# Kernel optimization log

Hardware: AMD Instinct MI355X
Metric: run time of the kernel (lower is better)

Reference implementation:

```python
import jax, jax.numpy as jnp
import numpy as np

T, B, IN, H, E = 100, 1, 36, 256, 2048


def setup_inputs() -> dict:
    key = jax.random.key(0)
    ks = jax.random.split(key, 18)
    rn = lambda k, shape, s=1.0: jax.random.normal(k, shape, jnp.float32) * s
    return dict(
        Y=rn(ks[0], (T, B, IN)),
        h0=rn(ks[1], (1, B, H)),
        c0=rn(ks[2], (1, B, H)),
        outEncoder=rn(ks[3], (E, H), 0.1),
        W_ih=rn(ks[4], (4 * H, IN), 0.1),
        W_hh=rn(ks[5], (4 * H, H), 0.1),
        b_ih=rn(ks[6], (4 * H,), 0.1),
        b_hh=rn(ks[7], (4 * H,), 0.1),
        att_W=rn(ks[8], (H, H), 0.1),
        att_V=rn(ks[9], (H, H), 0.1),
        att_b=rn(ks[10], (H, 1), 0.1),
        att_vector=rn(ks[11], (1, H), 0.1),
        W1=rn(ks[12], (H, 2 * H), 0.1),
        b1=rn(ks[13], (H,), 0.1),
        W2=rn(ks[14], (H, H), 0.1),
        b2=rn(ks[15], (H,), 0.1),
        W3=rn(ks[16], (IN, H), 0.1),
        b3=rn(ks[17], (IN,), 0.1),
    )


def reference(Y, h0, c0, outEncoder, W_ih, W_hh, b_ih, b_hh,
              att_W, att_V, att_b, att_vector, W1, b1, W2, b2, W3, b3):
    h = jnp.squeeze(h0, 0)  # [B,H]
    c = jnp.squeeze(c0, 0)  # [B,H]
    # VOut = att_V @ outEncoder^T is timestep-invariant: precompute. [H,E]
    VOut = att_V @ outEncoder.T

    def step(carry, y):
        h, c = carry  # h: [B,H], c: [B,H] (context from prev step after step 0)
        gates = y @ W_ih.T + b_ih + h @ W_hh.T + b_hh  # [B,4H]
        i_g, f_g, g_g, o_g = jnp.split(gates, 4, axis=1)
        cLSTM = jax.nn.sigmoid(f_g) * c + jax.nn.sigmoid(i_g) * jnp.tanh(g_g)
        h_new = jax.nn.sigmoid(o_g) * jnp.tanh(cLSTM)  # [B,H]
        # additive attention: hidden expanded to every encoder position
        WS = att_W @ h_new.T  # [H,1], broadcasts over E columns
        Escore = jnp.tanh(WS + VOut + att_b)  # [H,E]
        scores = att_vector @ Escore  # [1,E]
        alpha = jax.nn.softmax(scores, axis=-1)  # [1,E]
        ctx = alpha @ outEncoder  # [1,H]
        # MLP on concat(new cell state, context)
        v = jnp.concatenate([cLSTM, ctx], axis=1)  # [1,2H]
        v = jax.nn.relu(v @ W1.T + b1)
        v = jax.nn.relu(v @ W2.T + b2)
        out = v @ W3.T + b3  # [1,36]
        # NB: original feeds the attention context back as the LSTM cell state
        return (h_new, ctx), out

    (_, c_final), outputs = jax.lax.scan(step, (h, c), Y)
    return outputs, c_final  # outputs: [100,1,36]
```

## Files before the change

### kernel.cpp

```cpp
#include <hip/hip_runtime.h>
#include <stdint.h>


static constexpr float    L2E = 1.44269504088896341f;
static constexpr float    K2  = 2.88539008177792681f;
static constexpr unsigned SPIN_LIMIT = 200000u;

static constexpr size_t OFF_BC   = 0;
static constexpr size_t OFF_YG   = 524288;
static constexpr size_t OFF_GRAW = 626688;
static constexpr size_t OFF_CRAW = 729088;
static constexpr size_t CRAW_CP  = 25600;
static constexpr size_t OFF_STOT = 831488;
static constexpr size_t OFF_CLH  = 831616;
static constexpr size_t OFF_V1   = 857216;
static constexpr size_t OFF_V2   = 882816;
static constexpr size_t OFF_SYNC = 908416;

__device__ __forceinline__ float exp2fast(float x){ return __builtin_amdgcn_exp2f(x); }
__device__ __forceinline__ float rcpfast(float x){ return __builtin_amdgcn_rcpf(x); }
__device__ __forceinline__ float sigf(float x){ return rcpfast(1.f + exp2fast(-x*L2E)); }
__device__ __forceinline__ float tanhfast(float x){
  float E = exp2fast(x*K2);
  return 1.f - 2.f*rcpfast(E + 1.f);
}
__device__ __forceinline__ unsigned short f2bf(float f){
  unsigned b = __float_as_uint(f);
  return (unsigned short)((b + 0x7FFFu + ((b>>16)&1u))>>16);
}
__device__ __forceinline__ float bf2f(unsigned short u){ return __uint_as_float(((unsigned)u)<<16); }

__device__ __forceinline__ void gstore(float* p, float v){
  __hip_atomic_store(p, v, __ATOMIC_RELAXED, __HIP_MEMORY_SCOPE_AGENT);
}
__device__ __forceinline__ float gload(const float* p){
  return __hip_atomic_load(p, __ATOMIC_RELAXED, __HIP_MEMORY_SCOPE_AGENT);
}
__device__ __forceinline__ void gstore_u32(unsigned* p, unsigned v){
  __hip_atomic_store(p, v, __ATOMIC_RELAXED, __HIP_MEMORY_SCOPE_AGENT);
}
__device__ __forceinline__ unsigned gload_u32(const unsigned* p){
  return __hip_atomic_load(p, __ATOMIC_RELAXED, __HIP_MEMORY_SCOPE_AGENT);
}
__device__ __forceinline__ void gatomic_addf(float* p, float v){
  (void)__hip_atomic_fetch_add(p, v, __ATOMIC_RELAXED, __HIP_MEMORY_SCOPE_AGENT);
}

__device__ __forceinline__ void fbar(unsigned* flags, int w, unsigned ep){
  asm volatile("s_waitcnt vmcnt(0)" ::: "memory");
  __syncthreads();
  if (threadIdx.x == 0) gstore_u32(&flags[w], ep);
  if (threadIdx.x < 64) {
    int lane = threadIdx.x;
    unsigned it = 0;
    for (;;) {
      unsigned v = (lane < 32) ? gload_u32(&flags[lane]) : ep;
      if (__all((int)(v >= ep))) break;
      if (++it > SPIN_LIMIT) break;
    }
  }
  __syncthreads();
}
__device__ __forceinline__ void fwait_sleep(unsigned* flags, unsigned ep){
  if (threadIdx.x < 64) {
    int lane = threadIdx.x;
    unsigned it = 0;
    for (;;) {
      unsigned v = (lane < 32) ? gload_u32(&flags[lane]) : ep;
      if (__all((int)(v >= ep))) break;
      __builtin_amdgcn_s_sleep(2);
      if (++it > SPIN_LIMIT) break;
    }
  }
  __syncthreads();
}
__device__ __forceinline__ void arrive_cnt(unsigned* cnt){
  asm volatile("s_waitcnt vmcnt(0)" ::: "memory");
  __syncthreads();
  if (threadIdx.x == 0)
    __hip_atomic_fetch_add(cnt, 1u, __ATOMIC_RELAXED, __HIP_MEMORY_SCOPE_AGENT);
}
__device__ __forceinline__ void poll_ge(unsigned* p, unsigned tgt){
  if (threadIdx.x == 0){
    unsigned it = 0;
    while (gload_u32(p) < tgt){
      __builtin_amdgcn_s_sleep(2);
      if (++it > SPIN_LIMIT) break;
    }
  }
  __syncthreads();
}

__global__ __launch_bounds__(256) void rnn_prep(
    const float* __restrict__ Y, const float* __restrict__ h0,
    const float* __restrict__ outE, const float* __restrict__ W_ih,
    const float* __restrict__ W_hh, const float* __restrict__ b_ih,
    const float* __restrict__ b_hh, const float* __restrict__ att_V,
    const float* __restrict__ att_b, float* __restrict__ ws)
{
  __shared__ float avT[32*257];
  __shared__ float oeL[8*257];
  __shared__ float yL[40];
  __shared__ float h0L[256];
  const int b = blockIdx.x, tid = threadIdx.x;
  float* ws_bc   = ws + OFF_BC;
  float* ws_yg   = ws + OFF_YG;
  float* ws_graw = ws + OFF_GRAW;

  if (b < 256) {
    int e0 = b*8;
    for (int r=0;r<8;r++) oeL[r*257 + tid] = outE[(size_t)(e0+r)*256 + tid];
    int hl = tid & 31, er = tid >> 5;
    for (int ht=0; ht<8; ++ht) {
      __syncthreads();
      for (int i=0;i<32;i++){ int lin = tid + i*256; int r = lin>>8, j = lin&255;
        avT[r*257 + j] = att_V[(size_t)(ht*32+r)*256 + j]; }
      __syncthreads();
      float acc = 0.f;
      for (int j=0;j<256;j++) acc = fmaf(avT[hl*257 + j], oeL[er*257 + j], acc);
      int h = ht*32 + hl;
      ws_bc[(size_t)(e0+er)*256 + h] = (acc + att_b[h]) * K2;
    }
  } else if (b < 260) {
    int g = b - 256;
    for (int u=0; u<25; ++u) {
      int t = g*25 + u;
      __syncthreads();
      if (tid < 36) yL[tid] = Y[t*36 + tid];
      __syncthreads();
      for (int q=0;q<4;q++){
        int i = tid + 256*q;
        float acc = b_ih[i] + b_hh[i];
        for (int j=0;j<36;j++) acc = fmaf(W_ih[(size_t)i*36 + j], yL[j], acc);
        ws_yg[(size_t)t*1024 + i] = acc;
      }
    }
  } else if (b < 292) {
    int s = b - 260;
    if (tid < 256) h0L[tid] = h0[tid];
    if (tid < 36)  yL[tid]  = Y[tid];
    __syncthreads();
    int r = tid>>3, l8 = tid&7;
    int R = s*32 + r;
    float acc = 0.f;
    for (int q=0;q<32;q++){ int j = l8*32 + q; acc = fmaf(W_hh[(size_t)R*256 + j], h0L[j], acc); }
    acc += __shfl_xor(acc,1); acc += __shfl_xor(acc,2); acc += __shfl_xor(acc,4);
    if (l8 == 0){
      float full = acc + b_ih[R] + b_hh[R];
      for (int j=0;j<36;j++) full = fmaf(W_ih[(size_t)R*36 + j], yL[j], full);
      ws_graw[R] = full;
    }
  } else if (b == 292) {
    unsigned* s0 = (unsigned*)(ws + OFF_SYNC);
    gstore_u32(&s0[tid], 0u); gstore_u32(&s0[tid + 256], 0u);
  } else if (b == 293) {
    if (tid < 128) gstore(&ws[OFF_STOT + tid], 0.f);
  } else {
    int t = b - 294;
    #pragma unroll
    for (int c=0;c<4;c++)
      gstore(&ws[OFF_CRAW + (size_t)c*CRAW_CP + (size_t)t*256 + tid], 0.f);
  }
}

__global__ __launch_bounds__(512, 2) void rnn_main(
    const float* __restrict__ c0, const float* __restrict__ outE,
    const float* __restrict__ W_hh, const float* __restrict__ att_W,
    const float* __restrict__ att_vec,
    const float* __restrict__ W1, const float* __restrict__ b1,
    const float* __restrict__ W2, const float* __restrict__ b2,
    const float* __restrict__ W3, const float* __restrict__ b3,
    float* __restrict__ out, float* __restrict__ ws)
{
  __shared__ __align__(16) unsigned char smem[140288];
  const int w = blockIdx.x;
  const int tid = threadIdx.x;

  float* ws_yg    = ws + OFF_YG;
  float* ws_graw  = ws + OFF_GRAW;
  float* ws_craw  = ws + OFF_CRAW;
  float* ws_stot  = ws + OFF_STOT;
  float* ws_clh   = ws + OFF_CLH;
  float* ws_v1    = ws + OFF_V1;
  float* ws_v2    = ws + OFF_V2;
  unsigned* flags = (unsigned*)(ws + OFF_SYNC);
  unsigned* fv1   = flags + 64;
  unsigned* fv2   = flags + 192;

  if (w < 32) {
    float*          bcS    = (float*)(smem);
    unsigned short* oeS    = (unsigned short*)(smem + 67584);
    float*          whhS   = (float*)(smem + 100352);
    float*          wsS    = (float*)(smem + 133632);
    float*          hS     = (float*)(smem + 134688);
    float*          scoreS = (float*)(smem + 135712);
    float*          wexpS  = (float*)(smem + 135968);
    float*          pS     = (float*)(smem + 136224);
    float*          avS    = (float*)(smem + 138272);
    float*          stS    = (float*)(smem + 139328);

    unsigned awP[64];
    { int r = tid>>1, p = tid&1;
      const float* arow = att_W + (size_t)r*256 + p*128;
      #pragma unroll
      for (int q=0;q<64;q++){
        unsigned lo = f2bf(arow[2*q]);
        unsigned hi = f2bf(arow[2*q+1]);
        awP[q] = lo | (hi<<16);
      } }
    float Vpart = 0.f;
    { int l8 = tid & 7;
      #pragma unroll
      for (int k=0;k<32;k++) Vpart += att_vec[l8*32 + k]; }

    const float* ws_bc = ws + OFF_BC;
    for (int i=0;i<32;i++){ int lin = tid + i*512; int col = lin>>8, h = lin&255;
      bcS[col*264 + h + (h>>5)] = ws_bc[(size_t)(w*64+col)*256 + h]; }
    for (int i=0;i<32;i++){ int lin = tid + i*512; int col = lin>>8, h = lin&255;
      oeS[col*256 + h] = f2bf(outE[(size_t)(w*64+col)*256 + h]); }
    for (int i=0;i<16;i++){ int lin = tid + i*512; int r = lin>>8, j = lin&255;
      whhS[r*260 + j] = W_hh[(size_t)(w*32+r)*256 + j]; }
    if (tid < 256) avS[tid + (tid>>5)] = -2.f * att_vec[tid];
    __syncthreads();

    for (int t = 0; t < 100; ++t) {
      float ig, fg, gg, og;
      float cr0, cr1, cr2, cr3, st;
      if (tid < 256) {
        const float* g = ws_graw + (size_t)t*1024;
        ig = gload(&g[tid]);     fg = gload(&g[256+tid]);
        gg = gload(&g[512+tid]); og = gload(&g[768+tid]);
        if (t > 0) {
          const float* cb = ws_craw + (size_t)(t-1)*256 + tid;
          cr0 = gload(cb);             cr1 = gload(cb + CRAW_CP);
          cr2 = gload(cb + 2*CRAW_CP); cr3 = gload(cb + 3*CRAW_CP);
          st  = gload(&ws_stot[t-1]);
        }
      }
      if (tid < 256) {
        float c;
        if (t == 0) c = c0[tid];
        else        c = ((cr0+cr1)+(cr2+cr3)) * rcpfast(st);
        float cl = sigf(fg)*c + sigf(ig)*tanhfast(gg);
        float hn = sigf(og)*tanhfast(cl);
        hS[tid] = hn;
        if (w == 0) gstore(&ws_clh[(size_t)t*256 + tid], cl);
      }
      __syncthreads();
      { int r = tid>>1, p = tid&1;
        const float4* h4 = (const float4*)(hS + p*128);
        float acc = 0.f;
        #pragma unroll
        for (int i=0;i<32;i++){
          float4 hv = h4[i];
          unsigned pk0 = awP[2*i], pk1 = awP[2*i+1];
          acc = fmaf(__uint_as_float(pk0<<16),          hv.x, acc);
          acc = fmaf(__uint_as_float(pk0 & 0xffff0000u), hv.y, acc);
          acc = fmaf(__uint_as_float(pk1<<16),          hv.z, acc);
          acc = fmaf(__uint_as_float(pk1 & 0xffff0000u), hv.w, acc);
        }
        acc += __shfl_xor(acc, 1);
        if (p == 0) wsS[r + (r>>5)] = acc * K2; }
      __syncthreads();
      { int col = tid >> 3, l8 = tid & 7;
        const float* bcR = bcS + col*264 + l8*33;
        const float* wsR = wsS + l8*33;
        const float* avR = avS + l8*33;
        float acc = Vpart;
        #pragma unroll
        for (int k=0;k<32;k++){
          float E = exp2fast(bcR[k] + wsR[k]);
          acc = fmaf(avR[k], rcpfast(E + 1.f), acc);
        }
        acc += __shfl_xor(acc,1); acc += __shfl_xor(acc,2); acc += __shfl_xor(acc,4);
        if (l8 == 0) scoreS[col] = acc; }
      __syncthreads();
      if (tid < 64) {
        float ev = exp2fast(scoreS[tid] * L2E);
        wexpS[tid] = ev;
        float s = ev;
        #pragma unroll
        for (int d=1; d<64; d<<=1) s += __shfl_xor(s, d);
        if (tid == 0) gatomic_addf(&ws_stot[t], s);
      }
      __syncthreads();
      { int h = tid & 255, half = tid >> 8;
        float accp = 0.f;
        #pragma unroll
        for (int i=0;i<32;i++){ int lc = half*32 + i;
          accp = fmaf(wexpS[lc], bf2f(oeS[lc*256 + h]), accp); }
        pS[half*256 + h] = accp; }
      __syncthreads();
      if (tid < 256)
        gatomic_addf(&ws_craw[(size_t)(w>>3)*CRAW_CP + (size_t)t*256 + tid],
                     pS[tid] + pS[256 + tid]);
      if (t <= 98) {
        int r32 = tid >> 4, l16 = tid & 15;
        float acc2 = 0.f;
        #pragma unroll
        for (int q=0;q<16;q++){ int j = l16 + 16*q; acc2 = fmaf(whhS[r32*260 + j], hS[j], acc2); }
        acc2 += __shfl_xor(acc2,1); acc2 += __shfl_xor(acc2,2);
        acc2 += __shfl_xor(acc2,4); acc2 += __shfl_xor(acc2,8);
        if (l16 == 0){ int R = w*32 + r32;
          gstore(&ws_graw[(size_t)(t+1)*1024 + R], acc2 + ws_yg[(size_t)(t+1)*1024 + R]); }
      }
      fbar(flags, w, (unsigned)(t+1));
    }
    if (w == 0 && tid < 256) {
      const float* cb = ws_craw + (size_t)99*256 + tid;
      float rsum = (gload(cb) + gload(cb + CRAW_CP))
                 + (gload(cb + 2*CRAW_CP) + gload(cb + 3*CRAW_CP));
      out[3600 + tid] = rsum * rcpfast(gload(&ws_stot[99]));
    }
  } else if (w < 36) {
    float* wmS = (float*)(smem);
    float* vbS = (float*)(smem + 133632);
    int m = w - 32;
    for (int i=0;i<64;i++){ int lin = tid + i*512; int r = lin>>9, k = lin&511;
      wmS[r*520 + k + (k>>6)] = W1[(size_t)(m*64+r)*512 + k]; }
    __syncthreads();
    for (int s=0; s<100; ++s){
      fwait_sleep(flags, (unsigned)(s+1));
      { float val;
        if (tid < 256) val = gload(&ws_clh[(size_t)s*256 + tid]);
        else {
          const float* cb = ws_craw + (size_t)s*256 + (tid-256);
          float rsum = (gload(cb) + gload(cb + CRAW_CP))
                     + (gload(cb + 2*CRAW_CP) + gload(cb + 3*CRAW_CP));
          val = rsum * rcpfast(gload(&ws_stot[s]));
        }
        vbS[tid + (tid>>6)] = val; }
      __syncthreads();
      int row = tid >> 3, l8 = tid & 7;
      const float* wr = wmS + row*520 + l8*65;
      const float* vr = vbS + l8*65;
      float acc = 0.f;
      #pragma unroll
      for (int q=0;q<64;q++) acc = fmaf(wr[q], vr[q], acc);
      acc += __shfl_xor(acc,1); acc += __shfl_xor(acc,2); acc += __shfl_xor(acc,4);
      if (l8 == 0){ int i = m*64 + row; gstore(&ws_v1[(size_t)s*256 + i], fmaxf(acc + b1[i], 0.f)); }
      arrive_cnt(&fv1[s]);
      __syncthreads();
    }
  } else if (w < 38) {
    float* wmS = (float*)(smem);
    float* vbS = (float*)(smem + 133632);
    int m = w - 36;
    for (int i=0;i<64;i++){ int lin = tid + i*512; int r = lin>>8, k = lin&255;
      wmS[r*260 + k + (k>>6)] = W2[(size_t)(m*128+r)*256 + k]; }
    __syncthreads();
    for (int s=0; s<100; ++s){
      poll_ge(&fv1[s], 4u);
      if (tid < 256) vbS[tid + (tid>>6)] = gload(&ws_v1[(size_t)s*256 + tid]);
      __syncthreads();
      int row = tid >> 2, l4 = tid & 3;
      const float* wr = wmS + row*260 + l4*65;
      const float* vr = vbS + l4*65;
      float acc = 0.f;
      #pragma unroll
      for (int q=0;q<64;q++) acc = fmaf(wr[q], vr[q], acc);
      acc += __shfl_xor(acc,1); acc += __shfl_xor(acc,2);
      if (l4 == 0){ int i = m*128 + row; gstore(&ws_v2[(size_t)s*256 + i], fmaxf(acc + b2[i], 0.f)); }
      arrive_cnt(&fv2[s]);
      __syncthreads();
    }
  } else {
    float* wmS = (float*)(smem);
    float* vbS = (float*)(smem + 37440);
    for (int lin = tid; lin < 36*256; lin += 512){ int r = lin>>8, k = lin&255;
      wmS[r*260 + k + (k>>6)] = W3[(size_t)r*256 + k]; }
    __syncthreads();
    for (int s=0; s<100; ++s){
      poll_ge(&fv2[s], 2u);
      if (tid < 256) vbS[tid + (tid>>6)] = gload(&ws_v2[(size_t)s*256 + tid]);
      __syncthreads();
      if (tid < 288) {
        int row = tid >> 3, l8 = tid & 7;
        int kb = l8*32;
        const float* wr = wmS + row*260 + kb + (kb>>6);
        const float* vr = vbS + kb + (kb>>6);
        float acc = 0.f;
        #pragma unroll
        for (int q=0;q<32;q++) acc = fmaf(wr[q], vr[q], acc);
        acc += __shfl_xor(acc,1); acc += __shfl_xor(acc,2); acc += __shfl_xor(acc,4);
        if (l8 == 0) out[s*36 + row] = acc + b3[row];
      }
      __syncthreads();
    }
  }
}

extern "C" void kernel_launch(void* const* d_in, const int* in_sizes, int n_in,
                              void* d_out, int out_size, void* d_ws, size_t ws_size,
                              hipStream_t stream) {
  (void)in_sizes; (void)n_in; (void)out_size; (void)ws_size;
  const float* Y       = (const float*)d_in[0];
  const float* h0      = (const float*)d_in[1];
  const float* c0      = (const float*)d_in[2];
  const float* outEnc  = (const float*)d_in[3];
  const float* W_ih    = (const float*)d_in[4];
  const float* W_hh    = (const float*)d_in[5];
  const float* b_ih    = (const float*)d_in[6];
  const float* b_hh    = (const float*)d_in[7];
  const float* att_W   = (const float*)d_in[8];
  const float* att_V   = (const float*)d_in[9];
  const float* att_b   = (const float*)d_in[10];
  const float* att_vec = (const float*)d_in[11];
  const float* W1      = (const float*)d_in[12];
  const float* b1      = (const float*)d_in[13];
  const float* W2      = (const float*)d_in[14];
  const float* b2      = (const float*)d_in[15];
  const float* W3      = (const float*)d_in[16];
  const float* b3      = (const float*)d_in[17];
  float* out = (float*)d_out;
  float* ws  = (float*)d_ws;

  rnn_prep<<<dim3(394), dim3(256), 0, stream>>>(Y, h0, outEnc, W_ih, W_hh, b_ih, b_hh,
                                                att_V, att_b, ws);
  rnn_main<<<dim3(39), dim3(512), 0, stream>>>(c0, outEnc, W_hh, att_W, att_vec,
                                               W1, b1, W2, b2, W3, b3, out, ws);
}
```

Measured before the change: 680.6 us.

## Fuse softmax denominators into sign-flipped barrier flags and hoist W_hh matvec

Replaces the epoch-counter grid barrier and the atomically accumulated softmax sum with per-block float slots. Each slot carries that block's partial exp-sum, and its sign flips every two steps so it also serves as a readiness flag. Consumers poll the 32 slots and reduce them locally, which removes one atomic and one flag round trip per timestep. The W_hh recurrent matvec for the next step now runs right after h is computed, and the cell-state write is spread across blocks. The double-buffered sign scheme depends on producers not running more than one step ahead of slow consumers.

```diff
diff --git a/kernel.cpp b/kernel.cpp
--- a/kernel.cpp
+++ b/kernel.cpp
@@ -11,7 +11,7 @@
 static constexpr size_t OFF_GRAW = 626688;
 static constexpr size_t OFF_CRAW = 729088;
 static constexpr size_t CRAW_CP  = 25600;
-static constexpr size_t OFF_STOT = 831488;
+static constexpr size_t OFF_FST  = 831488;
 static constexpr size_t OFF_CLH  = 831616;
 static constexpr size_t OFF_V1   = 857216;
 static constexpr size_t OFF_V2   = 882816;
@@ -46,33 +46,23 @@
   (void)__hip_atomic_fetch_add(p, v, __ATOMIC_RELAXED, __HIP_MEMORY_SCOPE_AGENT);
 }
 
-__device__ __forceinline__ void fbar(unsigned* flags, int w, unsigned ep){
-  asm volatile("s_waitcnt vmcnt(0)" ::: "memory");
-  __syncthreads();
-  if (threadIdx.x == 0) gstore_u32(&flags[w], ep);
-  if (threadIdx.x < 64) {
-    int lane = threadIdx.x;
-    unsigned it = 0;
-    for (;;) {
-      unsigned v = (lane < 32) ? gload_u32(&flags[lane]) : ep;
-      if (__all((int)(v >= ep))) break;
+__device__ __forceinline__ void poll_fst(const float* buf, bool pos, float* stS, bool polite){
+  if (threadIdx.x < 64){
+    float v; unsigned it = 0;
+    for(;;){
+      v = (threadIdx.x < 32) ? gload(&buf[threadIdx.x]) : (pos ? 1.f : -1.f);
+      bool ok = pos ? (v > 0.f) : (v < 0.f);
+      if (__all((int)ok)) break;
+      if (polite) __builtin_amdgcn_s_sleep(2);
       if (++it > SPIN_LIMIT) break;
     }
+    float s = (threadIdx.x < 32) ? fabsf(v) : 0.f;
+    #pragma unroll
+    for (int d=1; d<64; d<<=1) s += __shfl_xor(s, d);
+    if (threadIdx.x == 0) stS[0] = s;
   }
   __syncthreads();
-}
-__device__ __forceinline__ void fwait_sleep(unsigned* flags, unsigned ep){
-  if (threadIdx.x < 64) {
-    int lane = threadIdx.x;
-    unsigned it = 0;
-    for (;;) {
-      unsigned v = (lane < 32) ? gload_u32(&flags[lane]) : ep;
-      if (__all((int)(v >= ep))) break;
-      __builtin_amdgcn_s_sleep(2);
-      if (++it > SPIN_LIMIT) break;
-    }
-  }
-  __syncthreads();
+  asm volatile("" ::: "memory");
 }
 __device__ __forceinline__ void arrive_cnt(unsigned* cnt){
   asm volatile("s_waitcnt vmcnt(0)" ::: "memory");
@@ -89,6 +79,7 @@
     }
   }
   __syncthreads();
+  asm volatile("" ::: "memory");
 }
 
 __global__ __launch_bounds__(256) void rnn_prep(
@@ -154,7 +145,7 @@
     unsigned* s0 = (unsigned*)(ws + OFF_SYNC);
     gstore_u32(&s0[tid], 0u); gstore_u32(&s0[tid + 256], 0u);
   } else if (b == 293) {
-    if (tid < 128) gstore(&ws[OFF_STOT + tid], 0.f);
+    if (tid < 64) gstore(&ws[OFF_FST + tid], -1.0f);
   } else {
     int t = b - 294;
     #pragma unroll
@@ -179,13 +170,13 @@
   float* ws_yg    = ws + OFF_YG;
   float* ws_graw  = ws + OFF_GRAW;
   float* ws_craw  = ws + OFF_CRAW;
-  float* ws_stot  = ws + OFF_STOT;
+  float* fst      = ws + OFF_FST;
   float* ws_clh   = ws + OFF_CLH;
   float* ws_v1    = ws + OFF_V1;
   float* ws_v2    = ws + OFF_V2;
-  unsigned* flags = (unsigned*)(ws + OFF_SYNC);
-  unsigned* fv1   = flags + 64;
-  unsigned* fv2   = flags + 192;
+  unsigned* syncb = (unsigned*)(ws + OFF_SYNC);
+  unsigned* fv1   = syncb + 64;
+  unsigned* fv2   = syncb + 192;
 
   if (w < 32) {
     float*          bcS    = (float*)(smem);
@@ -224,29 +215,39 @@
     __syncthreads();
 
     for (int t = 0; t < 100; ++t) {
-      float ig, fg, gg, og;
-      float cr0, cr1, cr2, cr3, st;
+      if (t > 0) poll_fst(fst + ((t-1)&1)*32, ((((t-1)>>1)&1)==0), stS, false);
+      else       __syncthreads();
+      float ygn = 0.f;
+      int Rn = w*32 + (tid>>4);
+      if (t <= 98) ygn = ws_yg[(size_t)(t+1)*1024 + Rn];
       if (tid < 256) {
         const float* g = ws_graw + (size_t)t*1024;
-        ig = gload(&g[tid]);     fg = gload(&g[256+tid]);
-        gg = gload(&g[512+tid]); og = gload(&g[768+tid]);
-        if (t > 0) {
-          const float* cb = ws_craw + (size_t)(t-1)*256 + tid;
-          cr0 = gload(cb);             cr1 = gload(cb + CRAW_CP);
-          cr2 = gload(cb + 2*CRAW_CP); cr3 = gload(cb + 3*CRAW_CP);
-          st  = gload(&ws_stot[t-1]);
-        }
-      }
-      if (tid < 256) {
+        float ig = gload(&g[tid]);     float fg = gload(&g[256+tid]);
+        float gg = gload(&g[512+tid]); float og = gload(&g[768+tid]);
         float c;
         if (t == 0) c = c0[tid];
-        else        c = ((cr0+cr1)+(cr2+cr3)) * rcpfast(st);
+        else {
+          const float* cb = ws_craw + (size_t)(t-1)*256 + tid;
+          float cr0 = gload(cb);             float cr1 = gload(cb + CRAW_CP);
+          float cr2 = gload(cb + 2*CRAW_CP); float cr3 = gload(cb + 3*CRAW_CP);
+          c = ((cr0+cr1)+(cr2+cr3)) * rcpfast(stS[0]);
+        }
         float cl = sigf(fg)*c + sigf(ig)*tanhfast(gg);
         float hn = sigf(og)*tanhfast(cl);
         hS[tid] = hn;
-        if (w == 0) gstore(&ws_clh[(size_t)t*256 + tid], cl);
-      }
-      __syncthreads();
+        if ((tid>>3) == w) gstore(&ws_clh[(size_t)t*256 + tid], cl);
+      }
+      __syncthreads();
+      if (t <= 98) {
+        int l16 = tid & 15;
+        int r32 = tid >> 4;
+        float acc2 = 0.f;
+        #pragma unroll
+        for (int q=0;q<16;q++){ int j = l16 + 16*q; acc2 = fmaf(whhS[r32*260 + j], hS[j], acc2); }
+        acc2 += __shfl_xor(acc2,1); acc2 += __shfl_xor(acc2,2);
+        acc2 += __shfl_xor(acc2,4); acc2 += __shfl_xor(acc2,8);
+        if (l16 == 0) gstore(&ws_graw[(size_t)(t+1)*1024 + Rn], acc2 + ygn);
+      }
       { int r = tid>>1, p = tid&1;
         const float4* h4 = (const float4*)(hS + p*128);
         float acc = 0.f;
@@ -254,9 +255,9 @@
         for (int i=0;i<32;i++){
           float4 hv = h4[i];
           unsigned pk0 = awP[2*i], pk1 = awP[2*i+1];
-          acc = fmaf(__uint_as_float(pk0<<16),          hv.x, acc);
+          acc = fmaf(__uint_as_float(pk0<<16),           hv.x, acc);
           acc = fmaf(__uint_as_float(pk0 & 0xffff0000u), hv.y, acc);
-          acc = fmaf(__uint_as_float(pk1<<16),          hv.z, acc);
+          acc = fmaf(__uint_as_float(pk1<<16),           hv.z, acc);
           acc = fmaf(__uint_as_float(pk1 & 0xffff0000u), hv.w, acc);
         }
         acc += __shfl_xor(acc, 1);
@@ -275,13 +276,14 @@
         acc += __shfl_xor(acc,1); acc += __shfl_xor(acc,2); acc += __shfl_xor(acc,4);
         if (l8 == 0) scoreS[col] = acc; }
       __syncthreads();
+      float mySw = 0.f;
       if (tid < 64) {
         float ev = exp2fast(scoreS[tid] * L2E);
         wexpS[tid] = ev;
         float s = ev;
         #pragma unroll
         for (int d=1; d<64; d<<=1) s += __shfl_xor(s, d);
-        if (tid == 0) gatomic_addf(&ws_stot[t], s);
+        mySw = s;
       }
       __syncthreads();
       { int h = tid & 255, half = tid >> 8;
@@ -294,40 +296,39 @@
       if (tid < 256)
         gatomic_addf(&ws_craw[(size_t)(w>>3)*CRAW_CP + (size_t)t*256 + tid],
                      pS[tid] + pS[256 + tid]);
-      if (t <= 98) {
-        int r32 = tid >> 4, l16 = tid & 15;
-        float acc2 = 0.f;
-        #pragma unroll
-        for (int q=0;q<16;q++){ int j = l16 + 16*q; acc2 = fmaf(whhS[r32*260 + j], hS[j], acc2); }
-        acc2 += __shfl_xor(acc2,1); acc2 += __shfl_xor(acc2,2);
-        acc2 += __shfl_xor(acc2,4); acc2 += __shfl_xor(acc2,8);
-        if (l16 == 0){ int R = w*32 + r32;
-          gstore(&ws_graw[(size_t)(t+1)*1024 + R], acc2 + ws_yg[(size_t)(t+1)*1024 + R]); }
-      }
-      fbar(flags, w, (unsigned)(t+1));
-    }
-    if (w == 0 && tid < 256) {
-      const float* cb = ws_craw + (size_t)99*256 + tid;
-      float rsum = (gload(cb) + gload(cb + CRAW_CP))
-                 + (gload(cb + 2*CRAW_CP) + gload(cb + 3*CRAW_CP));
-      out[3600 + tid] = rsum * rcpfast(gload(&ws_stot[99]));
+      asm volatile("s_waitcnt vmcnt(0)" ::: "memory");
+      __syncthreads();
+      if (tid == 0) {
+        bool posT = (((t>>1)&1)==0);
+        gstore(&fst[(t&1)*32 + w], posT ? mySw : -mySw);
+      }
+    }
+    if (w == 0) {
+      poll_fst(fst + 32 , false , stS, false);
+      if (tid < 256) {
+        const float* cb = ws_craw + (size_t)99*256 + tid;
+        float rsum = (gload(cb) + gload(cb + CRAW_CP))
+                   + (gload(cb + 2*CRAW_CP) + gload(cb + 3*CRAW_CP));
+        out[3600 + tid] = rsum * rcpfast(stS[0]);
+      }
     }
   } else if (w < 36) {
-    float* wmS = (float*)(smem);
-    float* vbS = (float*)(smem + 133632);
+    float* wmS  = (float*)(smem);
+    float* vbS  = (float*)(smem + 133632);
+    float* stSm = (float*)(smem + 136000);
     int m = w - 32;
     for (int i=0;i<64;i++){ int lin = tid + i*512; int r = lin>>9, k = lin&511;
       wmS[r*520 + k + (k>>6)] = W1[(size_t)(m*64+r)*512 + k]; }
     __syncthreads();
     for (int s=0; s<100; ++s){
-      fwait_sleep(flags, (unsigned)(s+1));
+      poll_fst(fst + (s&1)*32, (((s>>1)&1)==0), stSm, true);
       { float val;
         if (tid < 256) val = gload(&ws_clh[(size_t)s*256 + tid]);
         else {
           const float* cb = ws_craw + (size_t)s*256 + (tid-256);
           float rsum = (gload(cb) + gload(cb + CRAW_CP))
                      + (gload(cb + 2*CRAW_CP) + gload(cb + 3*CRAW_CP));
-          val = rsum * rcpfast(gload(&ws_stot[s]));
+          val = rsum * rcpfast(stSm[0]);
         }
         vbS[tid + (tid>>6)] = val; }
       __syncthreads();
```

Measured after the change: 720.6 us. 1.06x slower.

## Replace float atomic accumulation of attention context with per-block partial buffers

Applied to the files above, without the earlier changes.

Each attention block now writes its partial context vector and softmax denominator into its own slot of a workspace buffer, replacing atomic adds into four shared copies. Consumers gather all 32 partials and reduce them in a fixed order. This removes atomic contention on the serial timestep path and the prep blocks that zeroed the accumulators. In exchange every reader issues 64 loads per element instead of 5. Launch bounds also change to one block per SM occupancy hint.

```diff
diff --git a/kernel.cpp b/kernel.cpp
--- a/kernel.cpp
+++ b/kernel.cpp
@@ -9,13 +9,12 @@
 static constexpr size_t OFF_BC   = 0;
 static constexpr size_t OFF_YG   = 524288;
 static constexpr size_t OFF_GRAW = 626688;
-static constexpr size_t OFF_CRAW = 729088;
-static constexpr size_t CRAW_CP  = 25600;
-static constexpr size_t OFF_STOT = 831488;
-static constexpr size_t OFF_CLH  = 831616;
-static constexpr size_t OFF_V1   = 857216;
-static constexpr size_t OFF_V2   = 882816;
-static constexpr size_t OFF_SYNC = 908416;
+static constexpr size_t OFF_PV   = 729088;
+static constexpr size_t PV_WG    = 26000;
+static constexpr size_t OFF_CLH  = 1561088;
+static constexpr size_t OFF_V1   = 1586688;
+static constexpr size_t OFF_V2   = 1612288;
+static constexpr size_t OFF_SYNC = 1637888;
 
 __device__ __forceinline__ float exp2fast(float x){ return __builtin_amdgcn_exp2f(x); }
 __device__ __forceinline__ float rcpfast(float x){ return __builtin_amdgcn_rcpf(x); }
@@ -41,9 +40,6 @@
 }
 __device__ __forceinline__ unsigned gload_u32(const unsigned* p){
   return __hip_atomic_load(p, __ATOMIC_RELAXED, __HIP_MEMORY_SCOPE_AGENT);
-}
-__device__ __forceinline__ void gatomic_addf(float* p, float v){
-  (void)__hip_atomic_fetch_add(p, v, __ATOMIC_RELAXED, __HIP_MEMORY_SCOPE_AGENT);
 }
 
 __device__ __forceinline__ void fbar(unsigned* flags, int w, unsigned ep){
@@ -89,6 +85,29 @@
     }
   }
   __syncthreads();
+}
+
+__device__ __forceinline__ float pv_combine(const float* ws_pv, int t, int h){
+  const float* pvb = ws_pv + (size_t)t*260 + h;
+  const float* smb = ws_pv + (size_t)t*260 + 256;
+  float pvv[32];
+  #pragma unroll
+  for (int i=0;i<32;i++) pvv[i] = gload(pvb + (size_t)i*PV_WG);
+  float s0=0.f,s1=0.f,s2=0.f,s3=0.f;
+  #pragma unroll
+  for (int i=0;i<8;i++){
+    s0 += gload(smb + (size_t)(4*i+0)*PV_WG);
+    s1 += gload(smb + (size_t)(4*i+1)*PV_WG);
+    s2 += gload(smb + (size_t)(4*i+2)*PV_WG);
+    s3 += gload(smb + (size_t)(4*i+3)*PV_WG);
+  }
+  float st = (s0+s1)+(s2+s3);
+  float a0=0.f,a1=0.f,a2=0.f,a3=0.f;
+  #pragma unroll
+  for (int i=0;i<8;i++){
+    a0 += pvv[4*i+0]; a1 += pvv[4*i+1]; a2 += pvv[4*i+2]; a3 += pvv[4*i+3];
+  }
+  return ((a0+a1)+(a2+a3)) * rcpfast(st);
 }
 
 __global__ __launch_bounds__(256) void rnn_prep(
@@ -150,20 +169,13 @@
       for (int j=0;j<36;j++) full = fmaf(W_ih[(size_t)R*36 + j], yL[j], full);
       ws_graw[R] = full;
     }
-  } else if (b == 292) {
+  } else {
     unsigned* s0 = (unsigned*)(ws + OFF_SYNC);
     gstore_u32(&s0[tid], 0u); gstore_u32(&s0[tid + 256], 0u);
-  } else if (b == 293) {
-    if (tid < 128) gstore(&ws[OFF_STOT + tid], 0.f);
-  } else {
-    int t = b - 294;
-    #pragma unroll
-    for (int c=0;c<4;c++)
-      gstore(&ws[OFF_CRAW + (size_t)c*CRAW_CP + (size_t)t*256 + tid], 0.f);
-  }
-}
-
-__global__ __launch_bounds__(512, 2) void rnn_main(
+  }
+}
+
+__global__ __launch_bounds__(512, 1) void rnn_main(
     const float* __restrict__ c0, const float* __restrict__ outE,
     const float* __restrict__ W_hh, const float* __restrict__ att_W,
     const float* __restrict__ att_vec,
@@ -178,8 +190,7 @@
 
   float* ws_yg    = ws + OFF_YG;
   float* ws_graw  = ws + OFF_GRAW;
-  float* ws_craw  = ws + OFF_CRAW;
-  float* ws_stot  = ws + OFF_STOT;
+  float* ws_pv    = ws + OFF_PV;
   float* ws_clh   = ws + OFF_CLH;
   float* ws_v1    = ws + OFF_V1;
   float* ws_v2    = ws + OFF_V2;
@@ -197,7 +208,6 @@
     float*          wexpS  = (float*)(smem + 135968);
     float*          pS     = (float*)(smem + 136224);
     float*          avS    = (float*)(smem + 138272);
-    float*          stS    = (float*)(smem + 139328);
 
     unsigned awP[64];
     { int r = tid>>1, p = tid&1;
@@ -224,23 +234,15 @@
     __syncthreads();
 
     for (int t = 0; t < 100; ++t) {
-      float ig, fg, gg, og;
-      float cr0, cr1, cr2, cr3, st;
+      float ig, fg, gg, og, c;
       if (tid < 256) {
         const float* g = ws_graw + (size_t)t*1024;
         ig = gload(&g[tid]);     fg = gload(&g[256+tid]);
         gg = gload(&g[512+tid]); og = gload(&g[768+tid]);
-        if (t > 0) {
-          const float* cb = ws_craw + (size_t)(t-1)*256 + tid;
-          cr0 = gload(cb);             cr1 = gload(cb + CRAW_CP);
-          cr2 = gload(cb + 2*CRAW_CP); cr3 = gload(cb + 3*CRAW_CP);
-          st  = gload(&ws_stot[t-1]);
-        }
+        if (t == 0) c = c0[tid];
+        else        c = pv_combine(ws_pv, t-1, tid);
       }
       if (tid < 256) {
-        float c;
-        if (t == 0) c = c0[tid];
-        else        c = ((cr0+cr1)+(cr2+cr3)) * rcpfast(st);
         float cl = sigf(fg)*c + sigf(ig)*tanhfast(gg);
         float hn = sigf(og)*tanhfast(cl);
         hS[tid] = hn;
@@ -254,9 +256,9 @@
         for (int i=0;i<32;i++){
           float4 hv = h4[i];
           unsigned pk0 = awP[2*i], pk1 = awP[2*i+1];
-          acc = fmaf(__uint_as_float(pk0<<16),          hv.x, acc);
+          acc = fmaf(__uint_as_float(pk0<<16),           hv.x, acc);
           acc = fmaf(__uint_as_float(pk0 & 0xffff0000u), hv.y, acc);
-          acc = fmaf(__uint_as_float(pk1<<16),          hv.z, acc);
+          acc = fmaf(__uint_as_float(pk1<<16),           hv.z, acc);
           acc = fmaf(__uint_as_float(pk1 & 0xffff0000u), hv.w, acc);
         }
         acc += __shfl_xor(acc, 1);
@@ -281,7 +283,7 @@
         float s = ev;
         #pragma unroll
         for (int d=1; d<64; d<<=1) s += __shfl_xor(s, d);
-        if (tid == 0) gatomic_addf(&ws_stot[t], s);
+        if (tid == 0) gstore(&ws_pv[(size_t)w*PV_WG + (size_t)t*260 + 256], s);
       }
       __syncthreads();
       { int h = tid & 255, half = tid >> 8;
@@ -292,8 +294,7 @@
         pS[half*256 + h] = accp; }
       __syncthreads();
       if (tid < 256)
-        gatomic_addf(&ws_craw[(size_t)(w>>3)*CRAW_CP + (size_t)t*256 + tid],
-                     pS[tid] + pS[256 + tid]);
+        gstore(&ws_pv[(size_t)w*PV_WG + (size_t)t*260 + tid], pS[tid] + pS[256 + tid]);
       if (t <= 98) {
         int r32 = tid >> 4, l16 = tid & 15;
         float acc2 = 0.f;
@@ -306,12 +307,8 @@
       }
       fbar(flags, w, (unsigned)(t+1));
     }
-    if (w == 0 && tid < 256) {
-      const float* cb = ws_craw + (size_t)99*256 + tid;
-      float rsum = (gload(cb) + gload(cb + CRAW_CP))
-                 + (gload(cb + 2*CRAW_CP) + gload(cb + 3*CRAW_CP));
-      out[3600 + tid] = rsum * rcpfast(gload(&ws_stot[99]));
-    }
+    if (w == 0 && tid < 256)
+      out[3600 + tid] = pv_combine(ws_pv, 99, tid);
   } else if (w < 36) {
     float* wmS = (float*)(smem);
     float* vbS = (float*)(smem + 133632);
@@ -323,12 +320,7 @@
       fwait_sleep(flags, (unsigned)(s+1));
       { float val;
         if (tid < 256) val = gload(&ws_clh[(size_t)s*256 + tid]);
-        else {
-          const float* cb = ws_craw + (size_t)s*256 + (tid-256);
-          float rsum = (gload(cb) + gload(cb + CRAW_CP))
-                     + (gload(cb + 2*CRAW_CP) + gload(cb + 3*CRAW_CP));
-          val = rsum * rcpfast(gload(&ws_stot[s]));
-        }
+        else           val = pv_combine(ws_pv, s, tid - 256);
         vbS[tid + (tid>>6)] = val; }
       __syncthreads();
       int row = tid >> 3, l8 = tid & 7;
@@ -415,7 +407,7 @@
   float* out = (float*)d_out;
   float* ws  = (float*)d_ws;
 
-  rnn_prep<<<dim3(394), dim3(256), 0, stream>>>(Y, h0, outEnc, W_ih, W_hh, b_ih, b_hh,
+  rnn_prep<<<dim3(293), dim3(256), 0, stream>>>(Y, h0, outEnc, W_ih, W_hh, b_ih, b_hh,
                                                 att_V, att_b, ws);
   rnn_main<<<dim3(39), dim3(512), 0, stream>>>(c0, outEnc, W_hh, att_W, att_vec,
                                                W1, b1, W2, b2, W3, b3, out, ws);
```

Result: slower. 961.1 us (+41.2%).
